# Optimization experiments

Hardware: AMD Instinct MI355X
Metric: run time of the kernel (lower is better)

Reference implementation:

```python
import jax, jax.numpy as jnp
import numpy as np

B, H, W, C = 4, 128, 128, 256
APL = 3  # anchors per location


def setup_inputs() -> dict:
    key = jax.random.key(0)
    ks = jax.random.split(key, 4)
    inputs = jax.random.normal(ks[0], (B, H, W, C), dtype=jnp.float32)
    # he_normal-ish scaled weights
    w_shared = jax.random.normal(ks[1], (3, 3, C, 512), dtype=jnp.float32) * (2.0 / (3 * 3 * C)) ** 0.5
    b_shared = jnp.zeros((512,), dtype=jnp.float32)
    w_cls = jax.random.normal(ks[2], (1, 1, 512, 2 * APL), dtype=jnp.float32) * (2.0 / 512) ** 0.5
    b_cls = jnp.zeros((2 * APL,), dtype=jnp.float32)
    w_delta = jax.random.normal(ks[3], (1, 1, 512, 4 * APL), dtype=jnp.float32) * (2.0 / 512) ** 0.5
    b_delta = jnp.zeros((4 * APL,), dtype=jnp.float32)
    return {"inputs": inputs, "w_shared": w_shared, "b_shared": b_shared,
            "w_cls": w_cls, "b_cls": b_cls, "w_delta": w_delta, "b_delta": b_delta}


def reference(inputs, w_shared, b_shared, w_cls, b_cls, w_delta, b_delta):
    # rpn_conv_shared: 3x3 SAME conv -> ReLU
    shared = jax.lax.conv_general_dilated(
        inputs, w_shared, window_strides=(1, 1), padding='SAME',
        dimension_numbers=('NHWC', 'HWIO', 'NHWC')) + b_shared
    shared = jax.nn.relu(shared)
    b = inputs.shape[0]
    # 1x1 convs are just per-pixel matmuls
    cls = jnp.einsum('bhwc,co->bhwo', shared, w_cls[0, 0]) + b_cls
    rpn_class_logits = cls.reshape(b, -1, 2)  # [B, num_anchors, 2]
    rpn_probs = jax.nn.softmax(rpn_class_logits, axis=-1)
    dlt = jnp.einsum('bhwc,co->bhwo', shared, w_delta[0, 0]) + b_delta
    rpn_deltas = dlt.reshape(b, -1, 4)  # [B, num_anchors, 4]
    return (rpn_class_logits, rpn_probs, rpn_deltas)
```

## Files before the change

### kernel.cpp

```cpp
#include <hip/hip_runtime.h>
#include <stdint.h>

#define BATCH 4
#define HH 128
#define WW 128
#define CIN 256
#define CO 512
#define HP 130
#define NPIX (BATCH*HH*WW)
#define LOGITS_N (NPIX*6)
#define DELTA_BASE (2*LOGITS_N)

typedef short bf16x8 __attribute__((ext_vector_type(8)));
typedef unsigned short u16x8 __attribute__((ext_vector_type(8)));
typedef float f32x4 __attribute__((ext_vector_type(4)));
typedef unsigned int u32;

__device__ __forceinline__ unsigned short f2bf(float f) {
    union { float f; unsigned int u; } v; v.f = f;
    return (unsigned short)((v.u + 0x7FFFu + ((v.u >> 16) & 1u)) >> 16);
}

__device__ __forceinline__ void gload16(const unsigned short* g, char* l) {
    __builtin_amdgcn_global_load_lds(
        (const __attribute__((address_space(1))) u32*)g,
        (__attribute__((address_space(3))) u32*)l, 16, 0, 0);
}

__global__ __launch_bounds__(256) void k_pad_convert(const float* __restrict__ in,
                                                     unsigned short* __restrict__ out) {
    size_t q = (size_t)blockIdx.x*256 + threadIdx.x;
    if (q >= (size_t)BATCH*HP*HP*64) return;
    int c4 = ((int)q & 63) * 4;
    int pix = (int)(q >> 6);
    int xx = pix % HP; int t = pix / HP; int yy = t % HP; int b = t / HP;
    ushort4 r = {0, 0, 0, 0};
    if (yy >= 1 && yy <= HH && xx >= 1 && xx <= WW) {
        const float4 v = *(const float4*)(in + (((size_t)(b*HH) + (yy-1))*WW + (xx-1))*CIN + c4);
        r.x = f2bf(v.x); r.y = f2bf(v.y); r.z = f2bf(v.z); r.w = f2bf(v.w);
    }
    *(ushort4*)(out + (size_t)pix*CIN + c4) = r;
}

__global__ __launch_bounds__(256) void k_wt_convert(const float* __restrict__ w,
                                                    unsigned short* __restrict__ wt) {
    int n = blockIdx.x % CO; int tap = blockIdx.x / CO;
    int c = threadIdx.x;
    wt[((size_t)tap*CO + n)*CIN + c] = f2bf(w[((size_t)tap*CIN + c)*CO + n]);
}

__global__ __launch_bounds__(512, 2) void k_main8(
    const unsigned short* __restrict__ in_p,
    const unsigned short* __restrict__ wt,
    const float* __restrict__ b_sh,
    const float* __restrict__ w_cls,
    const float* __restrict__ w_dlt,
    float* __restrict__ part)
{
    extern __shared__ char LDS[];

    const int tid  = threadIdx.x;
    const int lane = tid & 63, wave = tid >> 6;
    const int l15  = lane & 15, l4 = lane >> 4;
    const int wm   = wave >> 2, wn = wave & 3;

    const int bid   = ((blockIdx.x & 7) << 6) + (blockIdx.x >> 3);
    const int ntile = bid & 1, mtile = bid >> 1;
    const int n0 = ntile << 8;
    const int b  = mtile >> 6;
    const int y0 = (mtile & 63) * 2;

    const int rl0 = tid >> 3, pc0 = tid & 7;
    const int kc0 = pc0 ^ (rl0 & 7);
    const int off = rl0*256 + kc0*8;
    const int t16 = tid*16;

    int base_a[2], base_b[2];
    #pragma unroll
    for (int kk = 0; kk < 2; kk++) {
        int swz = ((kk*32 + l4*8)*2) ^ ((l15 & 7) << 4);
        base_a[kk] = (wm*128 + l15)*128 + swz;
        base_b[kk] = 32768 + (wn*64 + l15)*128 + swz;
    }

    f32x4 acc[8][4];
    const f32x4 zz = {0.f, 0.f, 0.f, 0.f};
    #pragma unroll
    for (int mi = 0; mi < 8; mi++)
        #pragma unroll
        for (int ni = 0; ni < 4; ni++) acc[mi][ni] = zz;

    {
        const unsigned short* gB0 = wt + (size_t)n0*256;
        const unsigned short* gA0 = in_p + ((size_t)(b*HP + y0))*HP*256;
        char* Ad0 = LDS; char* Bd0 = LDS + 32768;
        gload16(gB0 + off,          Bd0 + t16);
        gload16(gB0 + 16384 + off,  Bd0 + 8192 + t16);
        gload16(gB0 + 32768 + off,  Bd0 + 16384 + t16);
        gload16(gB0 + 49152 + off,  Bd0 + 24576 + t16);
        gload16(gA0 + off,          Ad0 + t16);
        gload16(gA0 + 33280 + off,  Ad0 + 16384 + t16);
        gload16(gA0 + 16384 + off,  Ad0 + 8192 + t16);
        gload16(gA0 + 49664 + off,  Ad0 + 24576 + t16);
    }
    asm volatile("s_waitcnt vmcnt(2)" ::: "memory");
    __builtin_amdgcn_sched_barrier(0);
    __builtin_amdgcn_s_barrier();
    __builtin_amdgcn_sched_barrier(0);

#define MFMA_Q(Q)                                                            \
    __builtin_amdgcn_s_setprio(1);                                           \
    _Pragma("unroll")                                                        \
    for (int kk = 0; kk < 2; kk++)                                           \
        _Pragma("unroll")                                                    \
        for (int mm = 0; mm < 2; mm++)                                       \
            _Pragma("unroll")                                                \
            for (int ni = 0; ni < 4; ni++)                                   \
                acc[2*(Q)+mm][ni] = __builtin_amdgcn_mfma_f32_16x16x32_bf16( \
                    aq[mm][kk], breg[ni][kk], acc[2*(Q)+mm][ni], 0, 0, 0);   \
    __builtin_amdgcn_s_setprio(0);

#define LOAD_AQ(Q)                                                           \
    _Pragma("unroll")                                                        \
    for (int kk = 0; kk < 2; kk++) {                                         \
        aq[0][kk] = *(const bf16x8*)(bufc + base_a[kk] + (2*(Q))*2048);      \
        aq[1][kk] = *(const bf16x8*)(bufc + base_a[kk] + (2*(Q)+1)*2048);    \
    }

    for (int s = 0; s < 36; ++s) {
        const int s1 = s + 1;
        const int tap1 = s1 >> 2, kq1 = s1 & 3;
        const int dy1 = (tap1*11) >> 5, dx1 = tap1 - dy1*3;
        const unsigned short* gA = in_p + ((size_t)((b*HP + y0 + dy1)*HP + dx1))*256 + kq1*64;
        const unsigned short* gB = wt + ((size_t)(tap1*512 + n0))*256 + kq1*64;
        const int cur = s & 1;
        const char* bufc = LDS + (cur << 16);
        char* Ad = LDS + ((cur ^ 1) << 16);
        char* Bd = Ad + 32768;
        const bool more = (s < 35);

        if (more) {
            gload16(gB + off,          Bd + t16);
            gload16(gB + 16384 + off,  Bd + 8192 + t16);
            gload16(gB + 32768 + off,  Bd + 16384 + t16);
            gload16(gB + 49152 + off,  Bd + 24576 + t16);
            gload16(gA + off,          Ad + t16);
            gload16(gA + 33280 + off,  Ad + 16384 + t16);
            gload16(gA + 16384 + off,  Ad + 8192 + t16);
            gload16(gA + 49664 + off,  Ad + 24576 + t16);
        }

        bf16x8 breg[4][2];
        #pragma unroll
        for (int kk = 0; kk < 2; kk++) {
            breg[0][kk] = *(const bf16x8*)(bufc + base_b[kk]);
            breg[1][kk] = *(const bf16x8*)(bufc + base_b[kk] + 2048);
            breg[2][kk] = *(const bf16x8*)(bufc + base_b[kk] + 4096);
            breg[3][kk] = *(const bf16x8*)(bufc + base_b[kk] + 6144);
        }
        bf16x8 aq[2][2];
        LOAD_AQ(0)
        MFMA_Q(0)
        LOAD_AQ(1)
        MFMA_Q(1)
        if (more) { asm volatile("s_waitcnt vmcnt(8)" ::: "memory"); }
        else      { asm volatile("s_waitcnt vmcnt(0)" ::: "memory"); }
        __builtin_amdgcn_sched_barrier(0);
        LOAD_AQ(2)
        MFMA_Q(2)
        LOAD_AQ(3)
        MFMA_Q(3)

        if (more) { asm volatile("s_waitcnt vmcnt(2)" ::: "memory"); }
        __builtin_amdgcn_sched_barrier(0);
        __builtin_amdgcn_s_barrier();
        __builtin_amdgcn_sched_barrier(0);
    }
#undef MFMA_Q
#undef LOAD_AQ

    float* shf = (float*)LDS;
    float* sW  = (float*)(LDS + 66560);
    for (int j = tid; j < 256*18; j += 512) {
        int c = j / 18, o = j - c*18;
        sW[c*20 + o] = (o < 6) ? w_cls[(size_t)(n0 + c)*6 + o]
                               : w_dlt[(size_t)(n0 + c)*12 + (o - 6)];
    }
    float bsh[4];
    #pragma unroll
    for (int ni = 0; ni < 4; ni++) bsh[ni] = b_sh[n0 + wn*64 + ni*16 + l15];

    float a18[18];
    #pragma unroll
    for (int o = 0; o < 18; o++) a18[o] = 0.f;
    const int rr = tid & 255, chalf = tid >> 8;
    __syncthreads();

    for (int p = 0; p < 4; ++p) {
        if (wn == p) {
            #pragma unroll
            for (int mi = 0; mi < 8; mi++)
                #pragma unroll
                for (int ni = 0; ni < 4; ni++) {
                    int colL = ni*16 + l15;
                    int row0 = wm*128 + mi*16 + l4*4;
                    f32x4 v = acc[mi][ni];
                    f32x4 sv;
                    #pragma unroll
                    for (int r = 0; r < 4; r++) sv[r] = fmaxf(v[r] + bsh[ni], 0.f);
                    *(f32x4*)(shf + colL*260 + row0) = sv;
                }
        }
        __syncthreads();
        #pragma unroll 4
        for (int i = 0; i < 32; i++) {
            int c = chalf*32 + i;
            float v = shf[c*260 + rr];
            const float* wrow = sW + (p*64 + c)*20;
            #pragma unroll
            for (int o = 0; o < 18; o++) a18[o] += v * wrow[o];
        }
        __syncthreads();
    }

    if (chalf == 1) {
        #pragma unroll
        for (int o = 0; o < 18; o++) shf[rr*18 + o] = a18[o];
    }
    __syncthreads();
    if (chalf == 0) {
        float* dst = part + ((size_t)ntile*NPIX + (size_t)mtile*256 + rr)*18;
        #pragma unroll
        for (int o = 0; o < 18; o++) dst[o] = a18[o] + shf[rr*18 + o];
    }
}

__global__ __launch_bounds__(256) void k_finalize_ws(const float* __restrict__ part,
                                                     float* __restrict__ out,
                                                     const float* __restrict__ b_cls,
                                                     const float* __restrict__ b_dlt) {
    int pix = blockIdx.x*256 + threadIdx.x;
    if (pix >= NPIX) return;
    float s[18];
    #pragma unroll
    for (int o = 0; o < 18; o++)
        s[o] = part[(size_t)pix*18 + o] + part[((size_t)NPIX + pix)*18 + o];
    float* lo = out + (size_t)pix*6;
    float* pr = out + (size_t)LOGITS_N + (size_t)pix*6;
    float* dl = out + (size_t)DELTA_BASE + (size_t)pix*12;
    #pragma unroll
    for (int a = 0; a < 3; a++) {
        float l0 = s[a*2]   + b_cls[a*2];
        float l1 = s[a*2+1] + b_cls[a*2+1];
        lo[a*2] = l0; lo[a*2+1] = l1;
        float m = fmaxf(l0, l1);
        float e0 = __expf(l0 - m), e1 = __expf(l1 - m);
        float inv = 1.f / (e0 + e1);
        pr[a*2] = e0*inv; pr[a*2+1] = e1*inv;
    }
    #pragma unroll
    for (int o = 0; o < 12; o++) dl[o] = s[6 + o] + b_dlt[o];
}

__global__ __launch_bounds__(256) void k_main_fb(
    const float* __restrict__ in_f, const float* __restrict__ w_f,
    const float* __restrict__ b_sh, const float* __restrict__ w_cls,
    const float* __restrict__ w_dlt, float* __restrict__ out)
{
    __shared__ float smemf[11008];
    char* smem  = (char*)smemf;
    char* smemB = smem + 16384;
    const int tid = threadIdx.x;
    const int lane = tid & 63, wave = tid >> 6;
    const int l15 = lane & 15, l4 = lane >> 4;
    const int wr = wave >> 1, wc = wave & 1;
    int bid = ((blockIdx.x & 7) << 8) + (blockIdx.x >> 3);
    const int ntile = bid & 3, mtile = bid >> 2;
    const int n0 = ntile << 7;
    const int b = mtile >> 7, y = mtile & 127;
    int aoff[4][2], boff[4][2];
    #pragma unroll
    for (int mi = 0; mi < 4; mi++) {
        int rowA = wr*64 + mi*16 + l15;
        int rowB = wc*64 + mi*16 + l15;
        #pragma unroll
        for (int kk = 0; kk < 2; kk++) {
            int kb = (kk*32 + l4*8) * 2;
            aoff[mi][kk] = rowA*128 + (kb ^ ((rowA & 7) << 4));
            boff[mi][kk] = rowB*128 + (kb ^ ((rowB & 7) << 4));
        }
    }
    f32x4 acc[4][4];
    const f32x4 zz = {0.f, 0.f, 0.f, 0.f};
    #pragma unroll
    for (int mi = 0; mi < 4; mi++)
        #pragma unroll
        for (int ni = 0; ni < 4; ni++) acc[mi][ni] = zz;
    for (int s = 0; s < 36; s++) {
        int tap = s >> 2, kq = s & 3;
        int dy = tap / 3, dx = tap - dy*3;
        const int c0 = kq * 64;
        const int yy = y + dy - 1;
        const bool yok = (yy >= 0) && (yy < HH);
        #pragma unroll
        for (int i = 0; i < 4; i++) {
            int ci = i*256 + tid;
            int row = ci >> 3, pc = ci & 7;
            int kc = pc ^ (row & 7);
            int xx = row + dx - 1;
            u16x8 a;
            if (yok && xx >= 0 && xx < WW) {
                const float* sp = in_f + (((size_t)(b*HH) + yy)*WW + xx)*CIN + c0 + kc*8;
                #pragma unroll
                for (int j = 0; j < 8; j++) a[j] = (short)f2bf(sp[j]);
            } else {
                #pragma unroll
                for (int j = 0; j < 8; j++) a[j] = 0;
            }
            *(u16x8*)(smem + ci*16) = a;
            const float* wsrc = w_f + ((size_t)(tap*CIN + c0 + kc*8))*CO + n0 + row;
            u16x8 bb;
            #pragma unroll
            for (int j = 0; j < 8; j++) bb[j] = (short)f2bf(wsrc[(size_t)j*CO]);
            *(u16x8*)(smemB + ci*16) = bb;
        }
        __syncthreads();
        #pragma unroll
        for (int kk = 0; kk < 2; kk++) {
            bf16x8 av[4], bv[4];
            #pragma unroll
            for (int mi = 0; mi < 4; mi++) av[mi] = *(const bf16x8*)(smem  + aoff[mi][kk]);
            #pragma unroll
            for (int ni = 0; ni < 4; ni++) bv[ni] = *(const bf16x8*)(smemB + boff[ni][kk]);
            #pragma unroll
            for (int mi = 0; mi < 4; mi++)
                #pragma unroll
                for (int ni = 0; ni < 4; ni++)
                    acc[mi][ni] = __builtin_amdgcn_mfma_f32_16x16x32_bf16(
                        av[mi], bv[ni], acc[mi][ni], 0, 0, 0);
        }
        __syncthreads();
    }
    float* shf = smemf;
    float* sW  = smemf + 8448;
    for (int j = tid; j < 128*18; j += 256) {
        int c = j / 18, o = j - c*18;
        sW[c*20 + o] = (o < 6) ? w_cls[(size_t)(n0 + c)*6 + o]
                               : w_dlt[(size_t)(n0 + c)*12 + (o - 6)];
    }
    float bsh[4];
    #pragma unroll
    for (int ni = 0; ni < 4; ni++) bsh[ni] = b_sh[n0 + wc*64 + ni*16 + l15];
    float a18[18];
    #pragma unroll
    for (int o = 0; o < 18; o++) a18[o] = 0.f;
    const int rr = tid & 127, chalf = tid >> 7;
    #pragma unroll
    for (int pass = 0; pass < 2; pass++) {
        if (wc == pass) {
            #pragma unroll
            for (int mi = 0; mi < 4; mi++)
                #pragma unroll
                for (int ni = 0; ni < 4; ni++) {
                    int colL = ni*16 + l15;
                    int row0 = wr*64 + mi*16 + l4*4;
                    f32x4 v = acc[mi][ni];
                    f32x4 sv;
                    #pragma unroll
                    for (int r = 0; r < 4; r++) sv[r] = fmaxf(v[r] + bsh[ni], 0.f);
                    *(f32x4*)(shf + colL*132 + row0) = sv;
                }
        }
        __syncthreads();
        #pragma unroll 4
        for (int i = 0; i < 32; i++) {
            int c = chalf*32 + i;
            float v = shf[c*132 + rr];
            const float* wrow = sW + (pass*64 + c)*20;
            #pragma unroll
            for (int o = 0; o < 18; o++) a18[o] += v * wrow[o];
        }
        __syncthreads();
    }
    const int pixel = mtile*128 + rr;
    float* lo = out + (size_t)pixel*6;
    float* dl = out + DELTA_BASE + (size_t)pixel*12;
    #pragma unroll
    for (int o = 0; o < 6; o++)  atomicAdd(lo + o, a18[o]);
    #pragma unroll
    for (int o = 0; o < 12; o++) atomicAdd(dl + o, a18[6 + o]);
}

__global__ __launch_bounds__(256) void k_finalize(float* __restrict__ out,
                                                  const float* __restrict__ b_cls,
                                                  const float* __restrict__ b_dlt) {
    int pix = blockIdx.x*256 + threadIdx.x;
    if (pix >= NPIX) return;
    float* lo = out + (size_t)pix*6;
    float* pr = out + (size_t)LOGITS_N + (size_t)pix*6;
    float* dl = out + (size_t)DELTA_BASE + (size_t)pix*12;
    #pragma unroll
    for (int a = 0; a < 3; a++) {
        float l0 = lo[a*2]   + b_cls[a*2];
        float l1 = lo[a*2+1] + b_cls[a*2+1];
        lo[a*2] = l0; lo[a*2+1] = l1;
        float m = fmaxf(l0, l1);
        float e0 = __expf(l0 - m), e1 = __expf(l1 - m);
        float inv = 1.f / (e0 + e1);
        pr[a*2] = e0*inv; pr[a*2+1] = e1*inv;
    }
    #pragma unroll
    for (int o = 0; o < 12; o++) dl[o] += b_dlt[o];
}

extern "C" void kernel_launch(void* const* d_in, const int* in_sizes, int n_in,
                              void* d_out, int out_size, void* d_ws, size_t ws_size,
                              hipStream_t stream) {
    const float* in    = (const float*)d_in[0];
    const float* w_sh  = (const float*)d_in[1];
    const float* b_sh  = (const float*)d_in[2];
    const float* w_cls = (const float*)d_in[3];
    const float* b_cls = (const float*)d_in[4];
    const float* w_dlt = (const float*)d_in[5];
    const float* b_dlt = (const float*)d_in[6];
    float* out = (float*)d_out;

    const size_t in_p_elems = (size_t)BATCH*HP*HP*CIN;
    const size_t wt_elems   = (size_t)9*CO*CIN;
    const size_t part_elems = (size_t)2*NPIX*18;
    const size_t need = (in_p_elems + wt_elems)*2 + part_elems*4;

    if (ws_size >= need) {
        unsigned short* in_p = (unsigned short*)d_ws;
        unsigned short* wt   = in_p + in_p_elems;
        float* part = (float*)(wt + wt_elems);
        hipFuncSetAttribute((const void*)k_main8,
                            hipFuncAttributeMaxDynamicSharedMemorySize, 131072);
        int padq = (int)(((size_t)BATCH*HP*HP*64 + 255)/256);
        k_pad_convert<<<padq, 256, 0, stream>>>(in, in_p);
        k_wt_convert<<<9*CO, 256, 0, stream>>>(w_sh, wt);
        k_main8<<<512, 512, 131072, stream>>>(in_p, wt, b_sh, w_cls, w_dlt, part);
        k_finalize_ws<<<(NPIX + 255)/256, 256, 0, stream>>>(part, out, b_cls, b_dlt);
    } else {
        hipMemsetAsync(d_out, 0, (size_t)out_size * sizeof(float), stream);
        k_main_fb<<<2048, 256, 0, stream>>>(in, w_sh, b_sh, w_cls, w_dlt, out);
        k_finalize<<<(NPIX + 255)/256, 256, 0, stream>>>(out, b_cls, b_dlt);
    }
}
```

Baseline: 198.0 us.

## Split K-step into four barrier-synced phases interleaving global prefetch with MFMA

Restructures the main conv GEMM loop into four phases, each loading a slice of A/B fragments from LDS, issuing two of the eight async global-to-LDS loads, then syncing the workgroup with s_barrier before a block of MFMAs. The aim is to spread prefetch issue across the iteration and keep waves in lockstep, in the style of a ping-pong schedule, so that memory and matrix work overlap better. It adds two barriers per phase (eight per step), which risks extra synchronisation stalls. It also changes the register footprint, since B fragments are now held for one k-half at a time.

New measurement: 200.8 us. Within noise of the previous version (+1.4%).

```diff
diff --git a/kernel.cpp b/kernel.cpp
--- a/kernel.cpp
+++ b/kernel.cpp
@@ -108,23 +108,33 @@
     __builtin_amdgcn_s_barrier();
     __builtin_amdgcn_sched_barrier(0);
 
-#define MFMA_Q(Q)                                                            \
-    __builtin_amdgcn_s_setprio(1);                                           \
-    _Pragma("unroll")                                                        \
-    for (int kk = 0; kk < 2; kk++)                                           \
-        _Pragma("unroll")                                                    \
-        for (int mm = 0; mm < 2; mm++)                                       \
-            _Pragma("unroll")                                                \
-            for (int ni = 0; ni < 4; ni++)                                   \
-                acc[2*(Q)+mm][ni] = __builtin_amdgcn_mfma_f32_16x16x32_bf16( \
-                    aq[mm][kk], breg[ni][kk], acc[2*(Q)+mm][ni], 0, 0, 0);   \
-    __builtin_amdgcn_s_setprio(0);
-
-#define LOAD_AQ(Q)                                                           \
-    _Pragma("unroll")                                                        \
-    for (int kk = 0; kk < 2; kk++) {                                         \
-        aq[0][kk] = *(const bf16x8*)(bufc + base_a[kk] + (2*(Q))*2048);      \
-        aq[1][kk] = *(const bf16x8*)(bufc + base_a[kk] + (2*(Q)+1)*2048);    \
+#define PHASE(KK, MH, STAGE_CODE, WAIT_CODE)                                   \
+    {                                                                          \
+        bf16x8 aq[4];                                                          \
+        _Pragma("unroll")                                                      \
+        for (int j = 0; j < 4; j++)                                            \
+            aq[j] = *(const bf16x8*)(bufc + base_a[KK] + ((MH)*4 + j)*2048);   \
+        if ((MH) == 0) {                                                       \
+            _Pragma("unroll")                                                  \
+            for (int ni = 0; ni < 4; ni++)                                     \
+                breg[ni] = *(const bf16x8*)(bufc + base_b[KK] + ni*2048);      \
+        }                                                                      \
+        STAGE_CODE                                                             \
+        __builtin_amdgcn_sched_barrier(0);                                     \
+        __builtin_amdgcn_s_barrier();                                          \
+        asm volatile("s_waitcnt lgkmcnt(0)" ::: "memory");                     \
+        __builtin_amdgcn_sched_barrier(0);                                     \
+        __builtin_amdgcn_s_setprio(1);                                         \
+        _Pragma("unroll")                                                      \
+        for (int j = 0; j < 4; j++)                                            \
+            _Pragma("unroll")                                                  \
+            for (int ni = 0; ni < 4; ni++)                                     \
+                acc[(MH)*4 + j][ni] = __builtin_amdgcn_mfma_f32_16x16x32_bf16( \
+                    aq[j], breg[ni], acc[(MH)*4 + j][ni], 0, 0, 0);            \
+        __builtin_amdgcn_s_setprio(0);                                         \
+        WAIT_CODE                                                              \
+        __builtin_amdgcn_s_barrier();                                          \
+        __builtin_amdgcn_sched_barrier(0);                                     \
     }
 
     for (int s = 0; s < 36; ++s) {
@@ -139,45 +149,31 @@
         char* Bd = Ad + 32768;
         const bool more = (s < 35);
 
-        if (more) {
-            gload16(gB + off,          Bd + t16);
-            gload16(gB + 16384 + off,  Bd + 8192 + t16);
-            gload16(gB + 32768 + off,  Bd + 16384 + t16);
-            gload16(gB + 49152 + off,  Bd + 24576 + t16);
-            gload16(gA + off,          Ad + t16);
-            gload16(gA + 33280 + off,  Ad + 16384 + t16);
-            gload16(gA + 16384 + off,  Ad + 8192 + t16);
-            gload16(gA + 49664 + off,  Ad + 24576 + t16);
-        }
-
-        bf16x8 breg[4][2];
-        #pragma unroll
-        for (int kk = 0; kk < 2; kk++) {
-            breg[0][kk] = *(const bf16x8*)(bufc + base_b[kk]);
-            breg[1][kk] = *(const bf16x8*)(bufc + base_b[kk] + 2048);
-            breg[2][kk] = *(const bf16x8*)(bufc + base_b[kk] + 4096);
-            breg[3][kk] = *(const bf16x8*)(bufc + base_b[kk] + 6144);
-        }
-        bf16x8 aq[2][2];
-        LOAD_AQ(0)
-        MFMA_Q(0)
-        LOAD_AQ(1)
-        MFMA_Q(1)
-        if (more) { asm volatile("s_waitcnt vmcnt(8)" ::: "memory"); }
-        else      { asm volatile("s_waitcnt vmcnt(0)" ::: "memory"); }
-        __builtin_amdgcn_sched_barrier(0);
-        LOAD_AQ(2)
-        MFMA_Q(2)
-        LOAD_AQ(3)
-        MFMA_Q(3)
-
-        if (more) { asm volatile("s_waitcnt vmcnt(2)" ::: "memory"); }
-        __builtin_amdgcn_sched_barrier(0);
-        __builtin_amdgcn_s_barrier();
-        __builtin_amdgcn_sched_barrier(0);
-    }
-#undef MFMA_Q
-#undef LOAD_AQ
+        bf16x8 breg[4];
+
+        PHASE(0, 0,
+            if (more) { gload16(gB + off,         Bd + t16);
+                        gload16(gB + 16384 + off, Bd + 8192 + t16); },
+            if (more) { asm volatile("s_waitcnt vmcnt(2)" ::: "memory"); }
+            else      { asm volatile("s_waitcnt vmcnt(0)" ::: "memory"); }
+            __builtin_amdgcn_sched_barrier(0);
+        )
+        PHASE(0, 1,
+            if (more) { gload16(gB + 32768 + off, Bd + 16384 + t16);
+                        gload16(gB + 49152 + off, Bd + 24576 + t16); },
+        )
+        PHASE(1, 0,
+            if (more) { gload16(gA + off,         Ad + t16);
+                        gload16(gA + 33280 + off, Ad + 16384 + t16); },
+        )
+        PHASE(1, 1,
+            if (more) { gload16(gA + 16384 + off, Ad + 8192 + t16);
+                        gload16(gA + 49664 + off, Ad + 24576 + t16); },
+            if (more) { asm volatile("s_waitcnt vmcnt(2)" ::: "memory");
+                        __builtin_amdgcn_sched_barrier(0); }
+        )
+    }
+#undef PHASE
 
     float* shf = (float*)LDS;
     float* sW  = (float*)(LDS + 66560);
```

## Load B weights directly from global into registers, halve LDS footprint

Applied to the files above, without the earlier changes.

The weight (B) operand no longer goes through LDS. Each lane now reads its MFMA fragments straight from global memory into registers, double-buffered across the unrolled step pair with a prefetch of the next step. The LDS buffers now hold only the A tile, so dynamic shared memory drops from 128KB to about 85KB, which could allow more blocks per CU. The risks are higher register pressure and uncoalesced global loads of weights, plus tight vmcnt bookkeeping.

Result: slower. 380.3 us (+92.0%).

```diff
diff --git a/kernel.cpp b/kernel.cpp
--- a/kernel.cpp
+++ b/kernel.cpp
@@ -75,13 +75,14 @@
     const int off = rl0*256 + kc0*8;
     const int t16 = tid*16;
 
-    int base_a[2], base_b[2];
+    int base_a[2];
     #pragma unroll
     for (int kk = 0; kk < 2; kk++) {
         int swz = ((kk*32 + l4*8)*2) ^ ((l15 & 7) << 4);
         base_a[kk] = (wm*128 + l15)*128 + swz;
-        base_b[kk] = 32768 + (wn*64 + l15)*128 + swz;
-    }
+    }
+
+    const size_t bll = (size_t)(n0 + wn*64 + l15)*256 + l4*8;
 
     f32x4 acc[8][4];
     const f32x4 zz = {0.f, 0.f, 0.f, 0.f};
@@ -90,94 +91,103 @@
         #pragma unroll
         for (int ni = 0; ni < 4; ni++) acc[mi][ni] = zz;
 
+    bf16x8 X[4], Y[4];
+
     {
-        const unsigned short* gB0 = wt + (size_t)n0*256;
         const unsigned short* gA0 = in_p + ((size_t)(b*HP + y0))*HP*256;
-        char* Ad0 = LDS; char* Bd0 = LDS + 32768;
-        gload16(gB0 + off,          Bd0 + t16);
-        gload16(gB0 + 16384 + off,  Bd0 + 8192 + t16);
-        gload16(gB0 + 32768 + off,  Bd0 + 16384 + t16);
-        gload16(gB0 + 49152 + off,  Bd0 + 24576 + t16);
-        gload16(gA0 + off,          Ad0 + t16);
-        gload16(gA0 + 33280 + off,  Ad0 + 16384 + t16);
-        gload16(gA0 + 16384 + off,  Ad0 + 8192 + t16);
-        gload16(gA0 + 49664 + off,  Ad0 + 24576 + t16);
-    }
-    asm volatile("s_waitcnt vmcnt(2)" ::: "memory");
+        gload16(gA0 + off,          LDS + t16);
+        gload16(gA0 + 33280 + off,  LDS + 16384 + t16);
+        __builtin_amdgcn_sched_barrier(0);
+        gload16(gA0 + 16384 + off,  LDS + 8192 + t16);
+        gload16(gA0 + 49664 + off,  LDS + 24576 + t16);
+        __builtin_amdgcn_sched_barrier(0);
+        const unsigned short* gBX = wt + bll;
+        X[0] = *(const bf16x8*)(gBX);
+        X[1] = *(const bf16x8*)(gBX + 4096);
+        X[2] = *(const bf16x8*)(gBX + 8192);
+        X[3] = *(const bf16x8*)(gBX + 12288);
+        __builtin_amdgcn_sched_barrier(0);
+    }
+    asm volatile("s_waitcnt vmcnt(6)" ::: "memory");
     __builtin_amdgcn_sched_barrier(0);
     __builtin_amdgcn_s_barrier();
     __builtin_amdgcn_sched_barrier(0);
 
-#define MFMA_Q(Q)                                                            \
-    __builtin_amdgcn_s_setprio(1);                                           \
-    _Pragma("unroll")                                                        \
-    for (int kk = 0; kk < 2; kk++)                                           \
-        _Pragma("unroll")                                                    \
-        for (int mm = 0; mm < 2; mm++)                                       \
-            _Pragma("unroll")                                                \
-            for (int ni = 0; ni < 4; ni++)                                   \
-                acc[2*(Q)+mm][ni] = __builtin_amdgcn_mfma_f32_16x16x32_bf16( \
-                    aq[mm][kk], breg[ni][kk], acc[2*(Q)+mm][ni], 0, 0, 0);   \
+#define LOAD_QK(AQ, Q, KK)                                                     \
+    AQ[0] = *(const bf16x8*)(bufc + base_a[KK] + (2*(Q))*2048);                \
+    AQ[1] = *(const bf16x8*)(bufc + base_a[KK] + (2*(Q)+1)*2048);
+
+#define MFMA_QK(Q, AQ, BREG)                                                   \
+    __builtin_amdgcn_s_setprio(1);                                             \
+    _Pragma("unroll")                                                          \
+    for (int mm = 0; mm < 2; mm++)                                             \
+        _Pragma("unroll")                                                      \
+        for (int ni = 0; ni < 4; ni++)                                         \
+            acc[2*(Q)+mm][ni] = __builtin_amdgcn_mfma_f32_16x16x32_bf16(       \
+                AQ[mm], BREG[ni], acc[2*(Q)+mm][ni], 0, 0, 0);                 \
     __builtin_amdgcn_s_setprio(0);
 
-#define LOAD_AQ(Q)                                                           \
-    _Pragma("unroll")                                                        \
-    for (int kk = 0; kk < 2; kk++) {                                         \
-        aq[0][kk] = *(const bf16x8*)(bufc + base_a[kk] + (2*(Q))*2048);      \
-        aq[1][kk] = *(const bf16x8*)(bufc + base_a[kk] + (2*(Q)+1)*2048);    \
-    }
-
-    for (int s = 0; s < 36; ++s) {
-        const int s1 = s + 1;
-        const int tap1 = s1 >> 2, kq1 = s1 & 3;
-        const int dy1 = (tap1*11) >> 5, dx1 = tap1 - dy1*3;
-        const unsigned short* gA = in_p + ((size_t)((b*HP + y0 + dy1)*HP + dx1))*256 + kq1*64;
-        const unsigned short* gB = wt + ((size_t)(tap1*512 + n0))*256 + kq1*64;
-        const int cur = s & 1;
-        const char* bufc = LDS + (cur << 16);
-        char* Ad = LDS + ((cur ^ 1) << 16);
-        char* Bd = Ad + 32768;
-        const bool more = (s < 35);
-
-        if (more) {
-            gload16(gB + off,          Bd + t16);
-            gload16(gB + 16384 + off,  Bd + 8192 + t16);
-            gload16(gB + 32768 + off,  Bd + 16384 + t16);
-            gload16(gB + 49152 + off,  Bd + 24576 + t16);
-            gload16(gA + off,          Ad + t16);
-            gload16(gA + 33280 + off,  Ad + 16384 + t16);
-            gload16(gA + 16384 + off,  Ad + 8192 + t16);
-            gload16(gA + 49664 + off,  Ad + 24576 + t16);
-        }
-
-        bf16x8 breg[4][2];
-        #pragma unroll
-        for (int kk = 0; kk < 2; kk++) {
-            breg[0][kk] = *(const bf16x8*)(bufc + base_b[kk]);
-            breg[1][kk] = *(const bf16x8*)(bufc + base_b[kk] + 2048);
-            breg[2][kk] = *(const bf16x8*)(bufc + base_b[kk] + 4096);
-            breg[3][kk] = *(const bf16x8*)(bufc + base_b[kk] + 6144);
-        }
-        bf16x8 aq[2][2];
-        LOAD_AQ(0)
-        MFMA_Q(0)
-        LOAD_AQ(1)
-        MFMA_Q(1)
-        if (more) { asm volatile("s_waitcnt vmcnt(8)" ::: "memory"); }
-        else      { asm volatile("s_waitcnt vmcnt(0)" ::: "memory"); }
-        __builtin_amdgcn_sched_barrier(0);
-        LOAD_AQ(2)
-        MFMA_Q(2)
-        LOAD_AQ(3)
-        MFMA_Q(3)
-
-        if (more) { asm volatile("s_waitcnt vmcnt(2)" ::: "memory"); }
-        __builtin_amdgcn_sched_barrier(0);
-        __builtin_amdgcn_s_barrier();
-        __builtin_amdgcn_sched_barrier(0);
-    }
-#undef MFMA_Q
-#undef LOAD_AQ
+#define STEP_BODY(S, BC, BN)                                                   \
+{                                                                              \
+    const int s = (S);                                                         \
+    const bool more = (s < 35);                                                \
+    const int s1 = s + 1;                                                      \
+    const int tap1 = s1 >> 2, kq1 = s1 & 3;                                    \
+    const int dy1 = (tap1*11) >> 5, dx1 = tap1 - dy1*3;                        \
+    const int tap0 = s >> 2, kq0 = s & 3;                                      \
+    const unsigned short* gA  = in_p + ((size_t)((b*HP + y0 + dy1)*HP + dx1))*256 + kq1*64; \
+    const unsigned short* gBd = wt + bll + (size_t)tap0*131072 + kq0*64 + 32;  \
+    const unsigned short* gBn = wt + bll + (size_t)tap1*131072 + kq1*64;       \
+    const int cur = s & 1;                                                     \
+    const char* bufc = LDS + (cur << 15);                                      \
+    char* Ad = LDS + ((cur ^ 1) << 15);                                        \
+    bf16x8 a0[2], a1[2], a2[2], a3[2];                                         \
+    bf16x8 Bd[4];                                                              \
+    LOAD_QK(a0, 0, 0) LOAD_QK(a1, 1, 0)                                        \
+    __builtin_amdgcn_sched_barrier(0);                                         \
+    if (more) { gload16(gA + off,         Ad + t16);                           \
+                gload16(gA + 33280 + off, Ad + 16384 + t16); }                 \
+    __builtin_amdgcn_sched_barrier(0);                                         \
+    Bd[0] = *(const bf16x8*)(gBd);                                             \
+    Bd[1] = *(const bf16x8*)(gBd + 4096);                                      \
+    Bd[2] = *(const bf16x8*)(gBd + 8192);                                      \
+    Bd[3] = *(const bf16x8*)(gBd + 12288);                                     \
+    __builtin_amdgcn_sched_barrier(0);                                         \
+    if (more) { gload16(gA + 16384 + off, Ad + 8192 + t16);                    \
+                gload16(gA + 49664 + off, Ad + 24576 + t16); }                 \
+    __builtin_amdgcn_sched_barrier(0);                                         \
+    if (more) { BN[0] = *(const bf16x8*)(gBn);                                 \
+                BN[1] = *(const bf16x8*)(gBn + 4096);                          \
+                BN[2] = *(const bf16x8*)(gBn + 8192);                          \
+                BN[3] = *(const bf16x8*)(gBn + 12288); }                       \
+    __builtin_amdgcn_sched_barrier(0);                                         \
+    if (more) { asm volatile("s_waitcnt vmcnt(16)" ::: "memory"); }            \
+    else      { asm volatile("s_waitcnt vmcnt(8)"  ::: "memory"); }            \
+    __builtin_amdgcn_sched_barrier(0);                                         \
+    LOAD_QK(a2, 2, 0) LOAD_QK(a3, 3, 0)                                        \
+    MFMA_QK(0, a0, BC)                                                         \
+    MFMA_QK(1, a1, BC)                                                         \
+    MFMA_QK(2, a2, BC)                                                         \
+    bf16x8 c0[2], c1[2], c2[2], c3[2];                                         \
+    LOAD_QK(c0, 0, 1) LOAD_QK(c1, 1, 1)                                        \
+    LOAD_QK(c2, 2, 1) LOAD_QK(c3, 3, 1)                                        \
+    MFMA_QK(3, a3, BC)                                                         \
+    MFMA_QK(0, c0, Bd)                                                         \
+    MFMA_QK(1, c1, Bd)                                                         \
+    MFMA_QK(2, c2, Bd)                                                         \
+    MFMA_QK(3, c3, Bd)                                                         \
+    __builtin_amdgcn_sched_barrier(0);                                         \
+    __builtin_amdgcn_s_barrier();                                              \
+    __builtin_amdgcn_sched_barrier(0);                                         \
+}
+
+    for (int s2 = 0; s2 < 36; s2 += 2) {
+        STEP_BODY(s2,     X, Y)
+        STEP_BODY(s2 + 1, Y, X)
+    }
+#undef STEP_BODY
+#undef MFMA_QK
+#undef LOAD_QK
 
     float* shf = (float*)LDS;
     float* sW  = (float*)(LDS + 66560);
@@ -435,11 +445,11 @@
         unsigned short* wt   = in_p + in_p_elems;
         float* part = (float*)(wt + wt_elems);
         hipFuncSetAttribute((const void*)k_main8,
-                            hipFuncAttributeMaxDynamicSharedMemorySize, 131072);
+                            hipFuncAttributeMaxDynamicSharedMemorySize, 87040);
         int padq = (int)(((size_t)BATCH*HP*HP*64 + 255)/256);
         k_pad_convert<<<padq, 256, 0, stream>>>(in, in_p);
         k_wt_convert<<<9*CO, 256, 0, stream>>>(w_sh, wt);
-        k_main8<<<512, 512, 131072, stream>>>(in_p, wt, b_sh, w_cls, w_dlt, part);
+        k_main8<<<512, 512, 87040, stream>>>(in_p, wt, b_sh, w_cls, w_dlt, part);
         k_finalize_ws<<<(NPIX + 255)/256, 256, 0, stream>>>(part, out, b_cls, b_dlt);
     } else {
         hipMemsetAsync(d_out, 0, (size_t)out_size * sizeof(float), stream);
```
